# Performance work log

Hardware: AMD Instinct MI355X
Metric: run time of the kernel (lower is better)

## Reference

```python
import jax, jax.numpy as jnp
import numpy as np
import math

B, N, M, C, H = 8, 2048, 2048, 512, 8
DK = C // H
EPS_LN = 1e-5


def _layernorm(x, g, b):
    mu = jnp.mean(x, axis=-1, keepdims=True)
    var = jnp.var(x, axis=-1, keepdims=True)
    return (x - mu) / jnp.sqrt(var + EPS_LN) * g + b


def setup_inputs() -> dict:
    key = jax.random.key(0)
    ks = jax.random.split(key, 8)
    s = 0.02
    return {
        "cross_x": jax.random.normal(ks[0], (B, N, C), jnp.float32),
        "cross_y": jax.random.normal(ks[1], (B, M, C), jnp.float32),
        "ln_x_g": jnp.ones((C,), jnp.float32),
        "ln_x_b": jnp.zeros((C,), jnp.float32),
        "ln_y_g": jnp.ones((C,), jnp.float32),
        "ln_y_b": jnp.zeros((C,), jnp.float32),
        "Wq": jax.random.normal(ks[2], (C, C), jnp.float32) * s,
        "bq": jnp.zeros((C,), jnp.float32),
        "Wk": jax.random.normal(ks[3], (C, C), jnp.float32) * s,
        "bk": jnp.zeros((C,), jnp.float32),
        "Wv": jax.random.normal(ks[4], (C, C), jnp.float32) * s,
        "bv": jnp.zeros((C,), jnp.float32),
        "Wc": jax.random.normal(ks[5], (C, C), jnp.float32) * s,  # conv1x1 weight [out, in]
        "bc": jnp.zeros((C,), jnp.float32),
        "ln_o_g": jnp.ones((C,), jnp.float32),
        "ln_o_b": jnp.zeros((C,), jnp.float32),
    }


def reference(cross_x, cross_y, ln_x_g, ln_x_b, ln_y_g, ln_y_b,
              Wq, bq, Wk, bk, Wv, bv, Wc, bc, ln_o_g, ln_o_b):
    b, n, c = cross_x.shape
    m = cross_y.shape[1]
    xn = _layernorm(cross_x, ln_x_g, ln_x_b)
    yn = _layernorm(cross_y, ln_y_g, ln_y_b)
    # projections -> [B, H, seq, dk]
    q = (xn @ Wq + bq).reshape(b, n, H, DK).transpose(0, 2, 1, 3)
    k = (yn @ Wk + bk).reshape(b, m, H, DK).transpose(0, 2, 1, 3)
    v = (yn @ Wv + bv).reshape(b, m, H, DK).transpose(0, 2, 1, 3)
    scale = 1.0 / math.sqrt(DK)
    scores = jnp.einsum("bhnd,bhmd->bhnm", q, k) * scale
    attn = jax.nn.softmax(scores, axis=-1)
    # extra renormalization across the HEAD dimension (dim=1)
    attn = attn / (1e-9 + jnp.sum(attn, axis=1, keepdims=True))
    # dropout is identity in eval/reference mode
    o = jnp.einsum("bhnm,bhmd->bhnd", attn, v)
    q_flat = q.transpose(0, 2, 1, 3).reshape(b, n, c)  # [B, N, C]
    o_flat = o.transpose(0, 2, 1, 3).reshape(b, n, c)
    # conv1x1 over channels on (query - x)
    h = (q_flat - o_flat) @ Wc.T + bc
    h = jax.nn.leaky_relu(_layernorm(h, ln_o_g, ln_o_b), negative_slope=0.02)
    return q_flat + h
```

## Files before the change

### kernel.cpp

```cpp
#include <hip/hip_runtime.h>


typedef short bf16x8 __attribute__((ext_vector_type(8)));
typedef float f32x4 __attribute__((ext_vector_type(4)));
typedef float f32x2 __attribute__((ext_vector_type(2)));

#define CS 0.18033688f

__device__ inline float b2f(unsigned short u){
  union { unsigned int i; float f; } c; c.i = ((unsigned int)u) << 16; return c.f;
}
__device__ inline unsigned short f2b(float f){
  union { float ff; unsigned int i; } c; c.ff = f;
  unsigned int i = c.i;
  return (unsigned short)((i + 0x7FFFu + ((i >> 16) & 1u)) >> 16);
}
__device__ inline float fast_rcp(float x){ return __builtin_amdgcn_rcpf(x); }
__device__ inline f32x4 mfma16(bf16x8 a, bf16x8 b, f32x4 c){
  return __builtin_amdgcn_mfma_f32_16x16x32_bf16(a, b, c, 0, 0, 0);
}

__global__ void detect_dtype(const unsigned int* __restrict__ g, int* __restrict__ flag){
  *flag = (g[0] == 0x3F800000u) ? 1 : 0;
}

__global__ void zero_f32(float* __restrict__ p, int n){
  int i = blockIdx.x * 256 + threadIdx.x;
  if (i < n) p[i] = 0.0f;
}

__global__ void convert_misc(const void* Wc, const void* bq, const void* bk,
    const void* bv, const void* bc, const void* go, const void* bo,
    unsigned short* WcB, unsigned short* bqB, unsigned short* bkB,
    unsigned short* bvB, unsigned short* bcB, unsigned short* goB,
    unsigned short* boB, const int* __restrict__ flag){
  int i = blockIdx.x * 256 + threadIdx.x;
  const void* src; unsigned short* dst; int o;
  if (i < 262144){ src = Wc; dst = WcB; o = i; }
  else {
    int j = i - 262144; int seg = j >> 9; o = j & 511;
    if (seg == 0){ src = bq; dst = bqB; }
    else if (seg == 1){ src = bk; dst = bkB; }
    else if (seg == 2){ src = bv; dst = bvB; }
    else if (seg == 3){ src = bc; dst = bcB; }
    else if (seg == 4){ src = go; dst = goB; }
    else if (seg == 5){ src = bo; dst = boB; }
    else return;
  }
  if (*flag) dst[o] = f2b(((const float*)src)[o]);
  else       dst[o] = ((const unsigned short*)src)[o];
}

__global__ __launch_bounds__(128) void ln_rows(const void* __restrict__ xv,
    const void* __restrict__ gxv, const void* __restrict__ bxv,
    const void* __restrict__ yv, const void* __restrict__ gyv, const void* __restrict__ byv,
    unsigned short* __restrict__ outx, unsigned short* __restrict__ outy,
    const int* __restrict__ flag){
  int row = blockIdx.x & 16383;
  int sel = blockIdx.x >> 14;
  const void* src = sel ? yv : xv;
  const void* gv = sel ? gyv : gxv;
  const void* bv_ = sel ? byv : bxv;
  unsigned short* out = sel ? outy : outx;
  int t = threadIdx.x;
  float v0, v1, v2, v3, g0, g1, g2, g3, bb0, bb1, bb2, bb3;
  if (*flag){
    float4 xf = ((const float4*)((const float*)src + (size_t)row * 512))[t];
    v0 = xf.x; v1 = xf.y; v2 = xf.z; v3 = xf.w;
    float4 gf = ((const float4*)gv)[t];  g0 = gf.x; g1 = gf.y; g2 = gf.z; g3 = gf.w;
    float4 bf = ((const float4*)bv_)[t]; bb0 = bf.x; bb1 = bf.y; bb2 = bf.z; bb3 = bf.w;
  } else {
    ushort4 raw = ((const ushort4*)((const unsigned short*)src + (size_t)row * 512))[t];
    v0 = b2f(raw.x); v1 = b2f(raw.y); v2 = b2f(raw.z); v3 = b2f(raw.w);
    ushort4 gr = ((const ushort4*)gv)[t];  g0 = b2f(gr.x); g1 = b2f(gr.y); g2 = b2f(gr.z); g3 = b2f(gr.w);
    ushort4 br = ((const ushort4*)bv_)[t]; bb0 = b2f(br.x); bb1 = b2f(br.y); bb2 = b2f(br.z); bb3 = b2f(br.w);
  }
  float s = v0 + v1 + v2 + v3;
  float sq = v0*v0 + v1*v1 + v2*v2 + v3*v3;
  #pragma unroll
  for (int off = 32; off; off >>= 1){
    s += __shfl_down(s, off, 64);
    sq += __shfl_down(sq, off, 64);
  }
  __shared__ float red[4];
  if ((t & 63) == 0){ red[(t >> 6)*2] = s; red[(t >> 6)*2 + 1] = sq; }
  __syncthreads();
  s = red[0] + red[2]; sq = red[1] + red[3];
  float mu = s * (1.0f/512.0f);
  float rstd = rsqrtf(sq * (1.0f/512.0f) - mu*mu + 1e-5f);
  ushort4 o;
  o.x = f2b((v0 - mu)*rstd*g0 + bb0);
  o.y = f2b((v1 - mu)*rstd*g1 + bb1);
  o.z = f2b((v2 - mu)*rstd*g2 + bb2);
  o.w = f2b((v3 - mu)*rstd*g3 + bb3);
  ((ushort4*)(out + (size_t)row * 512))[t] = o;
}

__global__ __launch_bounds__(256) void transposeW(const void* __restrict__ wq,
    const void* __restrict__ wk, const void* __restrict__ wv,
    unsigned short* __restrict__ oq, unsigned short* __restrict__ ok,
    unsigned short* __restrict__ ov, const int* __restrict__ flag){
  __shared__ unsigned short tile[32][33];
  const void* in = (blockIdx.z == 0) ? wq : (blockIdx.z == 1) ? wk : wv;
  unsigned short* outp = (blockIdx.z == 0) ? oq : (blockIdx.z == 1) ? ok : ov;
  int k0 = blockIdx.x * 32, j0 = blockIdx.y * 32;
  int t = threadIdx.x;
  int r = t >> 3, c4 = (t & 7) * 4;
  if (*flag){
    float4 v = *(const float4*)((const float*)in + (size_t)(k0 + r) * 512 + j0 + c4);
    tile[r][c4] = f2b(v.x); tile[r][c4+1] = f2b(v.y);
    tile[r][c4+2] = f2b(v.z); tile[r][c4+3] = f2b(v.w);
  } else {
    ushort4 v = *(const ushort4*)((const unsigned short*)in + (size_t)(k0 + r) * 512 + j0 + c4);
    tile[r][c4] = v.x; tile[r][c4+1] = v.y; tile[r][c4+2] = v.z; tile[r][c4+3] = v.w;
  }
  __syncthreads();
  ushort4 o;
  o.x = tile[c4][r]; o.y = tile[c4+1][r]; o.z = tile[c4+2][r]; o.w = tile[c4+3][r];
  *(ushort4*)(outp + (size_t)(j0 + r) * 512 + k0 + c4) = o;
}

template<int OUT_MODE>
__global__ __launch_bounds__(256) void gemm_nt(const unsigned short* __restrict__ A,
    const unsigned short* __restrict__ Bt, const unsigned short* __restrict__ bias,
    void* __restrict__ Cout){
  __shared__ __align__(16) unsigned short As[128*32];
  __shared__ __align__(16) unsigned short Bs[128*32];
  int i0 = blockIdx.x * 128;
  int j0 = blockIdx.y * 128;
  int t = threadIdx.x;
  int w = t >> 6, lane = t & 63;
  int quad = lane >> 4, l15 = lane & 15;
  int wrow = (w >> 1) * 64, wcol = (w & 1) * 64;
  f32x4 acc[4][4];
  #pragma unroll
  for (int a = 0; a < 4; a++)
    #pragma unroll
    for (int b = 0; b < 4; b++)
      acc[a][b] = (f32x4){0.f, 0.f, 0.f, 0.f};

  int ra0 = t >> 2, ca0 = (t & 3) * 8;
  const unsigned short* Ag = A + (size_t)i0 * 512;
  const unsigned short* Bg = Bt + (size_t)j0 * 512;

  for (int kt = 0; kt < 16; kt++){
    int k0 = kt * 32;
    int4 av0 = *(const int4*)(Ag + (size_t)ra0 * 512 + k0 + ca0);
    int4 av1 = *(const int4*)(Ag + (size_t)(64 + ra0) * 512 + k0 + ca0);
    int4 bv0 = *(const int4*)(Bg + (size_t)ra0 * 512 + k0 + ca0);
    int4 bv1 = *(const int4*)(Bg + (size_t)(64 + ra0) * 512 + k0 + ca0);
    __syncthreads();
    ((int4*)As)[t] = av0; ((int4*)As)[t + 256] = av1;
    ((int4*)Bs)[t] = bv0; ((int4*)Bs)[t + 256] = bv1;
    __syncthreads();
    bf16x8 af[4], bfg[4];
    #pragma unroll
    for (int a = 0; a < 4; a++)
      af[a] = *(const bf16x8*)&As[(wrow + a*16 + l15)*32 + quad*8];
    #pragma unroll
    for (int b = 0; b < 4; b++)
      bfg[b] = *(const bf16x8*)&Bs[(wcol + b*16 + l15)*32 + quad*8];
    #pragma unroll
    for (int a = 0; a < 4; a++)
      #pragma unroll
      for (int b = 0; b < 4; b++)
        acc[a][b] = mfma16(af[a], bfg[b], acc[a][b]);
  }

  #pragma unroll
  for (int b = 0; b < 4; b++){
    int gcol = j0 + wcol + b*16 + l15;
    float bv = b2f(bias[gcol]);
    #pragma unroll
    for (int a = 0; a < 4; a++){
      #pragma unroll
      for (int r = 0; r < 4; r++){
        int grow = i0 + wrow + a*16 + quad*4 + r;
        float v = acc[a][b][r] + bv;
        if (OUT_MODE == 0){
          ((unsigned short*)Cout)[(size_t)grow*512 + gcol] = f2b(v);
        } else {
          int bb_ = grow >> 11, m = grow & 2047;
          int h = gcol >> 6, d = gcol & 63;
          ((unsigned short*)Cout)[((size_t)((bb_*8 + h)*64 + d))*2048 + m] = f2b(v);
        }
      }
    }
  }
}

__global__ __launch_bounds__(256) void attn_lsum(const unsigned short* __restrict__ Qm,
    const unsigned short* __restrict__ Km, float* __restrict__ Lsum){
  int wgl = blockIdx.x * 4 + (threadIdx.x >> 6);
  int b = wgl >> 9; int r_ = wgl & 511;
  int ntl = r_ >> 4; int ms = (r_ >> 2) & 3; int hg = r_ & 3;
  int h0 = hg * 2;
  int lane = threadIdx.x & 63, quad = lane >> 4, l15 = lane & 15;
  int n0 = ntl * 64;
  const unsigned short* Kp = Km + ((size_t)(b*2048)) * 512;
  bf16x8 aq[4][2][2];
  #pragma unroll
  for (int ns = 0; ns < 4; ns++)
    #pragma unroll
    for (int hh = 0; hh < 2; hh++)
      #pragma unroll
      for (int ks = 0; ks < 2; ks++)
        aq[ns][hh][ks] = *(const bf16x8*)(Qm + ((size_t)(b*2048 + n0 + ns*16 + l15))*512
                                          + (h0+hh)*64 + ks*32 + quad*8);
  float ls[4][2];
  #pragma unroll
  for (int ns = 0; ns < 4; ns++){ ls[ns][0] = 0.f; ls[ns][1] = 0.f; }
  for (int mt = 0; mt < 16; mt++){
    int m0 = ms*512 + mt*32;
    #pragma unroll
    for (int msub = 0; msub < 2; msub++){
      int mb = m0 + msub*16;
      #pragma unroll
      for (int hh = 0; hh < 2; hh++){
        bf16x8 ak0 = *(const bf16x8*)(Kp + (size_t)(mb + l15)*512 + (h0+hh)*64 + quad*8);
        bf16x8 ak1 = *(const bf16x8*)(Kp + (size_t)(mb + l15)*512 + (h0+hh)*64 + 32 + quad*8);
        #pragma unroll
        for (int ns = 0; ns < 4; ns++){
          f32x4 S = (f32x4){0.f,0.f,0.f,0.f};
          S = mfma16(ak0, aq[ns][hh][0], S);
          S = mfma16(ak1, aq[ns][hh][1], S);
          float e0 = exp2f(S[0]*CS), e1 = exp2f(S[1]*CS);
          float e2 = exp2f(S[2]*CS), e3 = exp2f(S[3]*CS);
          ls[ns][hh] += (e0 + e1) + (e2 + e3);
        }
      }
    }
  }
  #pragma unroll
  for (int ns = 0; ns < 4; ns++)
    #pragma unroll
    for (int hh = 0; hh < 2; hh++){
      float v = ls[ns][hh];
      v += __shfl_xor(v, 16, 64);
      v += __shfl_xor(v, 32, 64);
      ls[ns][hh] = v;
    }
  if (lane < 16){
    #pragma unroll
    for (int ns = 0; ns < 4; ns++)
      #pragma unroll
      for (int hh = 0; hh < 2; hh++)
        atomicAdd(&Lsum[(size_t)(b*8 + h0 + hh)*2048 + n0 + ns*16 + lane], ls[ns][hh]);
  }
}

__global__ __launch_bounds__(1024) void attn_out(const unsigned short* __restrict__ Qm,
    const unsigned short* __restrict__ Km, const unsigned short* __restrict__ VTm,
    const float* __restrict__ Lsum, unsigned short* __restrict__ DQO){
  __shared__ __align__(16) unsigned short Ks[32*512];
  __shared__ __align__(16) unsigned short Vs[512*40];
  __shared__ __align__(16) float ps[4][4*32*22];
  __shared__ __align__(16) unsigned short pb[4][8*16*40];
  int bid = blockIdx.x;
  int b = bid & 7;
  int ntl = bid >> 3;
  int t = threadIdx.x;
  int w = t >> 6;
  int hp = w & 3;
  int nsub = w >> 2;
  int lane = t & 63, quad = lane >> 4, l15 = lane & 15;
  int h0 = hp * 2;
  int n0 = ntl * 64 + nsub * 16;
  int kx = (l15 & 7) << 4;

  const unsigned short* Qp = Qm + ((size_t)(b*2048 + n0)) * 512;
  bf16x8 aq[2][2];
  #pragma unroll
  for (int hh = 0; hh < 2; hh++)
    #pragma unroll
    for (int ks = 0; ks < 2; ks++)
      aq[hh][ks] = *(const bf16x8*)(Qp + (size_t)l15*512 + (h0+hh)*64 + ks*32 + quad*8);
  float invl[2][4];
  #pragma unroll
  for (int hh = 0; hh < 2; hh++)
    #pragma unroll
    for (int r = 0; r < 4; r++)
      invl[hh][r] = fast_rcp(Lsum[(size_t)(b*8 + h0 + hh)*2048 + n0 + quad*4 + r]);
  f32x4 oacc[2][4];
  #pragma unroll
  for (int hh = 0; hh < 2; hh++)
    #pragma unroll
    for (int d = 0; d < 4; d++)
      oacc[hh][d] = (f32x4){0.f,0.f,0.f,0.f};

  const unsigned short* kg0 = Km + (size_t)b*1048576 + (size_t)(t>>6)*512 + (t&63)*8;
  const unsigned short* kg1 = kg0 + 16*512;
  const unsigned short* vg0 = VTm + (size_t)b*1048576 + (size_t)(t>>2)*2048 + (t&3)*8;
  const unsigned short* vg1 = vg0 + 256*2048;
  unsigned short* kl0 = Ks + (t>>6)*512 + (((((t&63)<<4)) ^ (((t>>6)&7)<<4)) >> 1);
  unsigned short* kl1 = kl0 + 16*512;
  unsigned short* vl0 = Vs + (t>>2)*40 + (t&3)*8;
  unsigned short* vl1 = vl0 + 256*40;

  int4 kA = *(const int4*)kg0, kB = *(const int4*)kg1;
  int4 vA = *(const int4*)vg0, vB = *(const int4*)vg1;

  float* psn = ps[nsub];
  unsigned short* pbn = pb[nsub];

  for (int mt = 0; mt < 64; mt++){
    *(int4*)kl0 = kA; *(int4*)kl1 = kB;
    *(int4*)vl0 = vA; *(int4*)vl1 = vB;
    __syncthreads();
    if (mt < 63){
      kg0 += 32*512; kg1 += 32*512; vg0 += 32; vg1 += 32;
      kA = *(const int4*)kg0; kB = *(const int4*)kg1;
      vA = *(const int4*)vg0; vB = *(const int4*)vg1;
    }
    float p[2][2][4];
    #pragma unroll
    for (int msub = 0; msub < 2; msub++){
      const char* kr = (const char*)Ks + (size_t)((msub*16 + l15) * 1024);
      #pragma unroll
      for (int hh = 0; hh < 2; hh++){
        int cb = (h0 + hh) * 128;
        bf16x8 k0 = *(const bf16x8*)(kr + ((cb + quad*16) ^ kx));
        bf16x8 k1 = *(const bf16x8*)(kr + ((cb + 64 + quad*16) ^ kx));
        f32x4 S = (f32x4){0.f,0.f,0.f,0.f};
        S = mfma16(aq[hh][0], k0, S);
        S = mfma16(aq[hh][1], k1, S);
        #pragma unroll
        for (int r = 0; r < 4; r++) p[hh][msub][r] = exp2f(S[r] * CS) * invl[hh][r];
      }
      int mb = hp*704 + (msub*16 + l15)*22 + quad*4;
      f32x2 s01 = {p[0][msub][0]+p[1][msub][0], p[0][msub][1]+p[1][msub][1]};
      f32x2 s23 = {p[0][msub][2]+p[1][msub][2], p[0][msub][3]+p[1][msub][3]};
      *(f32x2*)&psn[mb]     = s01;
      *(f32x2*)&psn[mb + 2] = s23;
    }
    __syncthreads();
    #pragma unroll
    for (int msub = 0; msub < 2; msub++){
      int mb = (msub*16 + l15)*22 + quad*4;
      f32x2 t01 = {1e-9f, 1e-9f}, t23 = {1e-9f, 1e-9f};
      #pragma unroll
      for (int hq = 0; hq < 4; hq++){
        t01 += *(const f32x2*)&psn[hq*704 + mb];
        t23 += *(const f32x2*)&psn[hq*704 + mb + 2];
      }
      float ir0 = fast_rcp(t01.x), ir1 = fast_rcp(t01.y);
      float ir2 = fast_rcp(t23.x), ir3 = fast_rcp(t23.y);
      #pragma unroll
      for (int hh = 0; hh < 2; hh++){
        int hb = (h0+hh)*640 + msub*16 + l15;
        pbn[hb + (quad*4+0)*40] = f2b(p[hh][msub][0] * ir0);
        pbn[hb + (quad*4+1)*40] = f2b(p[hh][msub][1] * ir1);
        pbn[hb + (quad*4+2)*40] = f2b(p[hh][msub][2] * ir2);
        pbn[hb + (quad*4+3)*40] = f2b(p[hh][msub][3] * ir3);
      }
    }
    #pragma unroll
    for (int hh = 0; hh < 2; hh++){
      bf16x8 wp = *(const bf16x8*)((const char*)pbn
                    + (size_t)((h0+hh)*1280 + l15*80) + quad*16);
      const char* vb = (const char*)Vs + (size_t)((((h0+hh)*64 + l15)) * 80) + quad*16;
      #pragma unroll
      for (int d = 0; d < 4; d++){
        bf16x8 vv = *(const bf16x8*)(vb + d*1280);
        oacc[hh][d] = mfma16(wp, vv, oacc[hh][d]);
      }
    }
    __syncthreads();
  }
  #pragma unroll
  for (int hh = 0; hh < 2; hh++){
    #pragma unroll
    for (int d = 0; d < 4; d++){
      #pragma unroll
      for (int r = 0; r < 4; r++){
        int n = n0 + quad*4 + r;
        int c = (h0+hh)*64 + d*16 + l15;
        size_t idx = ((size_t)(b*2048 + n))*512 + c;
        DQO[idx] = f2b(b2f(Qm[idx]) - oacc[hh][d][r]);
      }
    }
  }
}

__global__ __launch_bounds__(128) void finalize_k(const unsigned short* __restrict__ H,
    const unsigned short* __restrict__ Qb, const unsigned short* __restrict__ g,
    const unsigned short* __restrict__ bb, void* __restrict__ outp,
    const int* __restrict__ flag){
  int row = blockIdx.x; int t = threadIdx.x;
  ushort4 hraw = ((const ushort4*)(H + (size_t)row * 512))[t];
  float h0 = b2f(hraw.x), h1 = b2f(hraw.y), h2 = b2f(hraw.z), h3 = b2f(hraw.w);
  float s = h0 + h1 + h2 + h3;
  float sq = h0*h0 + h1*h1 + h2*h2 + h3*h3;
  #pragma unroll
  for (int off = 32; off; off >>= 1){
    s += __shfl_down(s, off, 64);
    sq += __shfl_down(sq, off, 64);
  }
  __shared__ float red[4];
  if ((t & 63) == 0){ red[(t >> 6)*2] = s; red[(t >> 6)*2 + 1] = sq; }
  __syncthreads();
  s = red[0] + red[2]; sq = red[1] + red[3];
  float mu = s * (1.0f/512.0f);
  float rstd = rsqrtf(sq * (1.0f/512.0f) - mu*mu + 1e-5f);
  ushort4 gr = ((const ushort4*)g)[t];
  ushort4 br = ((const ushort4*)bb)[t];
  ushort4 qr = ((const ushort4*)(Qb + (size_t)row * 512))[t];
  float y0 = (h0 - mu)*rstd*b2f(gr.x) + b2f(br.x); y0 = fmaxf(y0, 0.02f*y0);
  float y1 = (h1 - mu)*rstd*b2f(gr.y) + b2f(br.y); y1 = fmaxf(y1, 0.02f*y1);
  float y2 = (h2 - mu)*rstd*b2f(gr.z) + b2f(br.z); y2 = fmaxf(y2, 0.02f*y2);
  float y3 = (h3 - mu)*rstd*b2f(gr.w) + b2f(br.w); y3 = fmaxf(y3, 0.02f*y3);
  float o0 = b2f(qr.x) + y0, o1 = b2f(qr.y) + y1, o2 = b2f(qr.z) + y2, o3 = b2f(qr.w) + y3;
  if (*flag){
    float4 o; o.x = o0; o.y = o1; o.z = o2; o.w = o3;
    ((float4*)((float*)outp + (size_t)row * 512))[t] = o;
  } else {
    ushort4 o; o.x = f2b(o0); o.y = f2b(o1); o.z = f2b(o2); o.w = f2b(o3);
    ((ushort4*)((unsigned short*)outp + (size_t)row * 512))[t] = o;
  }
}

extern "C" void kernel_launch(void* const* d_in, const int* in_sizes, int n_in,
                              void* d_out, int out_size, void* d_ws, size_t ws_size,
                              hipStream_t stream){
  const void* x      = d_in[0];
  const void* y      = d_in[1];
  const void* ln_x_g = d_in[2];
  const void* ln_x_b = d_in[3];
  const void* ln_y_g = d_in[4];
  const void* ln_y_b = d_in[5];
  const void* Wq     = d_in[6];
  const void* bq     = d_in[7];
  const void* Wk     = d_in[8];
  const void* bk     = d_in[9];
  const void* Wv     = d_in[10];
  const void* bv     = d_in[11];
  const void* Wc     = d_in[12];
  const void* bc     = d_in[13];
  const void* ln_o_g = d_in[14];
  const void* ln_o_b = d_in[15];

  const size_t MB = (size_t)1 << 20;
  char* ws = (char*)d_ws;
  unsigned short* Qb  = (unsigned short*)(ws);
  unsigned short* Kb  = (unsigned short*)(ws + 16*MB);
  unsigned short* VT  = (unsigned short*)(ws + 32*MB);
  unsigned short* XN  = (unsigned short*)(ws + 48*MB);
  unsigned short* YN  = (unsigned short*)(ws + 64*MB);
  unsigned short* DQO = XN;
  unsigned short* Hpre = YN;
  unsigned short* WqT = (unsigned short*)(ws + 80*MB);
  unsigned short* WkT = WqT + 512*512;
  unsigned short* WvT = WkT + 512*512;
  unsigned short* WcB = WvT + 512*512;
  unsigned short* bqB = (unsigned short*)(ws + 82*MB);
  unsigned short* bkB = bqB + 512;
  unsigned short* bvB = bkB + 512;
  unsigned short* bcB = bvB + 512;
  unsigned short* goB = bcB + 512;
  unsigned short* boB = goB + 512;
  float* Lsum         = (float*)(ws + 83*MB);
  int* Flag           = (int*)(ws + 84*MB);

  detect_dtype<<<dim3(1), dim3(1), 0, stream>>>((const unsigned int*)ln_x_g, Flag);
  zero_f32<<<dim3(512), dim3(256), 0, stream>>>(Lsum, 131072);
  convert_misc<<<dim3(1037), dim3(256), 0, stream>>>(Wc, bq, bk, bv, bc, ln_o_g, ln_o_b,
      WcB, bqB, bkB, bvB, bcB, goB, boB, Flag);
  ln_rows<<<dim3(32768), dim3(128), 0, stream>>>(x, ln_x_g, ln_x_b, y, ln_y_g, ln_y_b,
      XN, YN, Flag);
  transposeW<<<dim3(16,16,3), dim3(256), 0, stream>>>(Wq, Wk, Wv, WqT, WkT, WvT, Flag);
  gemm_nt<0><<<dim3(128,4), dim3(256), 0, stream>>>(XN, WqT, bqB, (void*)Qb);
  gemm_nt<0><<<dim3(128,4), dim3(256), 0, stream>>>(YN, WkT, bkB, (void*)Kb);
  gemm_nt<2><<<dim3(128,4), dim3(256), 0, stream>>>(YN, WvT, bvB, (void*)VT);
  attn_lsum<<<dim3(1024), dim3(256), 0, stream>>>(Qb, Kb, Lsum);
  attn_out<<<dim3(256), dim3(1024), 0, stream>>>(Qb, Kb, VT, Lsum, DQO);
  gemm_nt<0><<<dim3(128,4), dim3(256), 0, stream>>>(DQO, WcB, bcB, (void*)Hpre);
  finalize_k<<<dim3(16384), dim3(128), 0, stream>>>(Hpre, Qb, goB, boB, d_out, Flag);
}
```

Measured before the change: 558.1 us.

## Load K fragments straight into registers and cut a barrier per tile in attn_out

The K tile is no longer staged through shared memory. Each wave loads its own bf16 K fragments from global memory into registers, prefetched one tile ahead. The V staging is reordered so the next tile's store happens after the second barrier, which removes one block-wide sync per iteration and uses explicit lgkmcnt barriers. The softmax normalisation now folds -log2(L) into the exp2 argument with an fma instead of multiplying by a reciprocal. The trade-off is that the four n-subtile wave groups each fetch the same K data from global/L2, so K traffic through the cache hierarchy goes up.

Measured after the change: 765.1 us. +37.1%, slower.

```diff
diff --git a/kernel.cpp b/kernel.cpp
--- a/kernel.cpp
+++ b/kernel.cpp
@@ -6,6 +6,11 @@
 typedef float f32x2 __attribute__((ext_vector_type(2)));
 
 #define CS 0.18033688f
+
+#define BARRIER_LG() do { __builtin_amdgcn_sched_barrier(0); \
+  asm volatile("s_waitcnt lgkmcnt(0)" ::: "memory"); \
+  __builtin_amdgcn_s_barrier(); \
+  __builtin_amdgcn_sched_barrier(0); } while(0)
 
 __device__ inline float b2f(unsigned short u){
   union { unsigned int i; float f; } c; c.i = ((unsigned int)u) << 16; return c.f;
@@ -252,7 +257,6 @@
 __global__ __launch_bounds__(1024) void attn_out(const unsigned short* __restrict__ Qm,
     const unsigned short* __restrict__ Km, const unsigned short* __restrict__ VTm,
     const float* __restrict__ Lsum, unsigned short* __restrict__ DQO){
-  __shared__ __align__(16) unsigned short Ks[32*512];
   __shared__ __align__(16) unsigned short Vs[512*40];
   __shared__ __align__(16) float ps[4][4*32*22];
   __shared__ __align__(16) unsigned short pb[4][8*16*40];
@@ -266,7 +270,6 @@
   int lane = t & 63, quad = lane >> 4, l15 = lane & 15;
   int h0 = hp * 2;
   int n0 = ntl * 64 + nsub * 16;
-  int kx = (l15 & 7) << 4;
 
   const unsigned short* Qp = Qm + ((size_t)(b*2048 + n0)) * 512;
   bf16x8 aq[2][2];
@@ -275,12 +278,12 @@
     #pragma unroll
     for (int ks = 0; ks < 2; ks++)
       aq[hh][ks] = *(const bf16x8*)(Qp + (size_t)l15*512 + (h0+hh)*64 + ks*32 + quad*8);
-  float invl[2][4];
+  float lg[2][4];
   #pragma unroll
   for (int hh = 0; hh < 2; hh++)
     #pragma unroll
     for (int r = 0; r < 4; r++)
-      invl[hh][r] = fast_rcp(Lsum[(size_t)(b*8 + h0 + hh)*2048 + n0 + quad*4 + r]);
+      lg[hh][r] = -log2f(Lsum[(size_t)(b*8 + h0 + hh)*2048 + n0 + quad*4 + r]);
   f32x4 oacc[2][4];
   #pragma unroll
   for (int hh = 0; hh < 2; hh++)
@@ -288,44 +291,40 @@
     for (int d = 0; d < 4; d++)
       oacc[hh][d] = (f32x4){0.f,0.f,0.f,0.f};
 
-  const unsigned short* kg0 = Km + (size_t)b*1048576 + (size_t)(t>>6)*512 + (t&63)*8;
-  const unsigned short* kg1 = kg0 + 16*512;
   const unsigned short* vg0 = VTm + (size_t)b*1048576 + (size_t)(t>>2)*2048 + (t&3)*8;
   const unsigned short* vg1 = vg0 + 256*2048;
-  unsigned short* kl0 = Ks + (t>>6)*512 + (((((t&63)<<4)) ^ (((t>>6)&7)<<4)) >> 1);
-  unsigned short* kl1 = kl0 + 16*512;
   unsigned short* vl0 = Vs + (t>>2)*40 + (t&3)*8;
-  unsigned short* vl1 = vl0 + 256*40;
-
-  int4 kA = *(const int4*)kg0, kB = *(const int4*)kg1;
+
   int4 vA = *(const int4*)vg0, vB = *(const int4*)vg1;
+  *(int4*)vl0 = vA; *(int4*)(vl0 + 10240) = vB;
+  vg0 += 32; vg1 += 32;
+  vA = *(const int4*)vg0; vB = *(const int4*)vg1;
+
+  const unsigned short* Kg = Km + (size_t)b*1048576;
+  int koff = l15*512 + quad*8;
+  bf16x8 kf[2][2][2];
+  #pragma unroll
+  for (int msub = 0; msub < 2; msub++)
+    #pragma unroll
+    for (int hh = 0; hh < 2; hh++)
+      #pragma unroll
+      for (int ks = 0; ks < 2; ks++)
+        kf[msub][hh][ks] = *(const bf16x8*)(Kg + koff + msub*8192 + (h0+hh)*64 + ks*32);
 
   float* psn = ps[nsub];
   unsigned short* pbn = pb[nsub];
 
   for (int mt = 0; mt < 64; mt++){
-    *(int4*)kl0 = kA; *(int4*)kl1 = kB;
-    *(int4*)vl0 = vA; *(int4*)vl1 = vB;
-    __syncthreads();
-    if (mt < 63){
-      kg0 += 32*512; kg1 += 32*512; vg0 += 32; vg1 += 32;
-      kA = *(const int4*)kg0; kB = *(const int4*)kg1;
-      vA = *(const int4*)vg0; vB = *(const int4*)vg1;
-    }
     float p[2][2][4];
     #pragma unroll
     for (int msub = 0; msub < 2; msub++){
-      const char* kr = (const char*)Ks + (size_t)((msub*16 + l15) * 1024);
       #pragma unroll
       for (int hh = 0; hh < 2; hh++){
-        int cb = (h0 + hh) * 128;
-        bf16x8 k0 = *(const bf16x8*)(kr + ((cb + quad*16) ^ kx));
-        bf16x8 k1 = *(const bf16x8*)(kr + ((cb + 64 + quad*16) ^ kx));
         f32x4 S = (f32x4){0.f,0.f,0.f,0.f};
-        S = mfma16(aq[hh][0], k0, S);
-        S = mfma16(aq[hh][1], k1, S);
+        S = mfma16(aq[hh][0], kf[msub][hh][0], S);
+        S = mfma16(aq[hh][1], kf[msub][hh][1], S);
         #pragma unroll
-        for (int r = 0; r < 4; r++) p[hh][msub][r] = exp2f(S[r] * CS) * invl[hh][r];
+        for (int r = 0; r < 4; r++) p[hh][msub][r] = exp2f(fmaf(S[r], CS, lg[hh][r]));
       }
       int mb = hp*704 + (msub*16 + l15)*22 + quad*4;
       f32x2 s01 = {p[0][msub][0]+p[1][msub][0], p[0][msub][1]+p[1][msub][1]};
@@ -333,7 +332,17 @@
       *(f32x2*)&psn[mb]     = s01;
       *(f32x2*)&psn[mb + 2] = s23;
     }
-    __syncthreads();
+    if (mt < 63){
+      Kg += 32*512;
+      #pragma unroll
+      for (int msub = 0; msub < 2; msub++)
+        #pragma unroll
+        for (int hh = 0; hh < 2; hh++)
+          #pragma unroll
+          for (int ks = 0; ks < 2; ks++)
+            kf[msub][hh][ks] = *(const bf16x8*)(Kg + koff + msub*8192 + (h0+hh)*64 + ks*32);
+    }
+    BARRIER_LG();
     #pragma unroll
     for (int msub = 0; msub < 2; msub++){
       int mb = (msub*16 + l15)*22 + quad*4;
@@ -365,7 +374,14 @@
         oacc[hh][d] = mfma16(wp, vv, oacc[hh][d]);
       }
     }
-    __syncthreads();
+    BARRIER_LG();
+    if (mt < 63){
+      *(int4*)vl0 = vA; *(int4*)(vl0 + 10240) = vB;
+      if (mt < 62){
+        vg0 += 32; vg1 += 32;
+        vA = *(const int4*)vg0; vB = *(const int4*)vg1;
+      }
+    }
   }
   #pragma unroll
   for (int hh = 0; hh < 2; hh++){
```
